# Performance work log

Hardware: AMD Instinct MI355X
Metric: run time of the kernel (lower is better)

## Reference

```python
import jax, jax.numpy as jnp
import numpy as np
from jax import lax

# Quantization bit-widths per the module: QuantAct(16) on input,
# QuantConv2d(precision[0]=8), QuantAct(precision[0]+3=11) after relu1,
# QuantLinear(precision[1]=8).
INPUT_BIT = 16
CONV_W_BIT = 8
RELU_BIT = 11
DENSE_W_BIT = 8
EPS = 1e-8


def round_ste(x):
    # straight-through estimator rounding (HAWQ SymmetricQuantFunction)
    return x + lax.stop_gradient(jnp.round(x) - x)


def quant_act(x, bit):
    """Per-tensor symmetric dynamic activation quantization (HAWQ QuantAct).
    Returns fake-quantized x and its scaling factor."""
    n = 2 ** (bit - 1) - 1
    scale = lax.stop_gradient(jnp.maximum(jnp.max(jnp.abs(x)), EPS) / n)
    x_q = jnp.clip(round_ste(x / scale), -n, n) * scale
    return x_q, scale


def quant_weight(w, bit):
    """Per-output-channel symmetric weight quantization. w: [out, ...].
    Returns integer-valued weights and per-channel scale [out]."""
    n = 2 ** (bit - 1) - 1
    absmax = jnp.max(jnp.abs(w.reshape(w.shape[0], -1)), axis=1)
    sf = lax.stop_gradient(jnp.maximum(absmax, EPS) / n)
    bshape = (w.shape[0],) + (1,) * (w.ndim - 1)
    w_int = jnp.clip(round_ste(w / sf.reshape(bshape)), -n, n)
    return w_int, sf


def quant_conv2d(x, p_sf, w, b, bit, stride, pad):
    w_int, w_sf = quant_weight(w, bit)          # [O,I,kh,kw], [O]
    x_int = x / p_sf                            # integer-valued activations
    out_int = lax.conv_general_dilated(
        x_int, w_int, window_strides=(stride, stride),
        padding=((pad, pad), (pad, pad)),
        dimension_numbers=("NCHW", "OIHW", "NCHW"))
    bias_sf = p_sf * w_sf                       # [O]
    b_int = round_ste(b / bias_sf)
    out = (out_int + b_int[None, :, None, None]) * bias_sf[None, :, None, None]
    return out, w_sf


def quant_linear(x, p_sf, w, b, bit):
    w_int, w_sf = quant_weight(w, bit)          # [O,I], [O]
    x_int = x / p_sf
    bias_sf = p_sf * w_sf                       # [O]
    b_int = round_ste(b / bias_sf)
    out = (jnp.einsum("bi,oi->bo", x_int, w_int) + b_int[None, :]) * bias_sf[None, :]
    return out


def setup_inputs() -> dict:
    key = jax.random.key(0)
    k1, k2, k3, k4, k5 = jax.random.split(key, 5)
    B, Cin, H, W = 256, 3, 64, 64
    Cout, K = 64, 3
    Fin, Fout = Cout * 32 * 32, 256  # stride-2 conv -> 32x32 spatial
    x = jax.random.normal(k1, (B, Cin, H, W), dtype=jnp.float32)
    conv_w = jax.random.normal(k2, (Cout, Cin, K, K), dtype=jnp.float32) * 0.1
    conv_b = jax.random.normal(k3, (Cout,), dtype=jnp.float32) * 0.01
    dense_w = jax.random.normal(k4, (Fout, Fin), dtype=jnp.float32) * 0.02
    dense_b = jax.random.normal(k5, (Fout,), dtype=jnp.float32) * 0.01
    return {"x": x, "conv_w": conv_w, "conv_b": conv_b,
            "dense_w": dense_w, "dense_b": dense_b}


def reference(x, conv_w, conv_b, dense_w, dense_b):
    # x, p_sf = quant_input(x)
    xq, p_sf = quant_act(x, INPUT_BIT)
    # x, w_sf = conv(x, p_sf)
    h, w_sf = quant_conv2d(xq, p_sf, conv_w, conv_b, CONV_W_BIT, stride=2, pad=1)
    # relu1
    h = jax.nn.relu(h)
    # x, p_sf = quant_relu(x, p_sf, w_sf)  (requantize at relu_bit)
    h, p_sf = quant_act(h, RELU_BIT)
    # flatten
    h = h.reshape(h.shape[0], -1)
    # relu2(enc_dense(x, p_sf))
    out = jax.nn.relu(quant_linear(h, p_sf, dense_w, dense_b, DENSE_W_BIT))
    return out
```

## Files before the change

kernel.cpp:

```cpp
#include <hip/hip_runtime.h>
#include <hip/hip_fp16.h>
#include <cstdint>

#define B_   256
#define CIN  3
#define HW_  64
#define COUT 64
#define FIN  65536
#define FOUT 256

#define ACC_F    0
#define SC_F     65536
#define XPART_F  65552
#define WPART_F  66064
#define CSF_F    67088
#define CWINT_F  67152
#define H16_BYTE (512*1024)
#define WQ_BYTE  (H16_BYTE + 256ll*FIN*2)

typedef _Float16 half8  __attribute__((ext_vector_type(8)));
typedef _Float16 half4v __attribute__((ext_vector_type(4)));
typedef float    floatx4 __attribute__((ext_vector_type(4)));
typedef unsigned short u16;
typedef unsigned int uint_;

__device__ inline float blockMax(float v) {
    #pragma unroll
    for (int off = 32; off; off >>= 1) v = fmaxf(v, __shfl_down(v, off));
    __shared__ float sm[8];
    const int lane = threadIdx.x & 63, w = threadIdx.x >> 6;
    if (lane == 0) sm[w] = v;
    __syncthreads();
    float m = sm[0];
    const int nw = blockDim.x >> 6;
    for (int i = 1; i < nw; i++) m = fmaxf(m, sm[i]);
    return m;
}

__global__ __launch_bounds__(256) void k_stats(const float* __restrict__ x,
                                               const float* __restrict__ dw,
                                               const float* __restrict__ cw,
                                               float* __restrict__ ws,
                                               signed char* __restrict__ wq) {
    const int b = blockIdx.x;
    const int t = threadIdx.x;
    if (b < 512) {
        const float4* x4 = (const float4*)x;
        float m = 0.f;
        for (int i = b * 256 + t; i < (B_ * CIN * HW_ * HW_) / 4; i += 512 * 256) {
            float4 v = x4[i];
            m = fmaxf(m, fmaxf(fmaxf(fabsf(v.x), fabsf(v.y)), fmaxf(fabsf(v.z), fabsf(v.w))));
        }
        float bm = blockMax(m);
        if (t == 0) ws[XPART_F + b] = bm;
    } else if (b < 768) {
        const int row = b - 512;
        const float4* r4 = (const float4*)(dw + (size_t)row * FIN);
        float m = 0.f;
        for (int i = t; i < FIN / 4; i += 256) {
            float4 v = r4[i];
            m = fmaxf(m, fmaxf(fmaxf(fabsf(v.x), fabsf(v.y)), fmaxf(fabsf(v.z), fabsf(v.w))));
        }
        const float am = blockMax(m);
        if (t == 0) ws[WPART_F + row] = am;
        const float inv = 127.0f / fmaxf(am, 1e-8f);
        uint_* wrow = (uint_*)(wq + (size_t)row * FIN);
        for (int i = t; i < FIN / 4; i += 256) {
            float4 v = r4[i];
            int q0 = (int)fminf(127.f, fmaxf(-127.f, rintf(v.x * inv)));
            int q1 = (int)fminf(127.f, fmaxf(-127.f, rintf(v.y * inv)));
            int q2 = (int)fminf(127.f, fmaxf(-127.f, rintf(v.z * inv)));
            int q3 = (int)fminf(127.f, fmaxf(-127.f, rintf(v.w * inv)));
            wrow[i] = (uint_)(q0 & 255) | ((uint_)(q1 & 255) << 8) |
                      ((uint_)(q2 & 255) << 16) | ((uint_)(q3 & 255) << 24);
        }
    } else if (b == 768) {
        if (t == 64) ((unsigned*)ws)[SC_F + 1] = 0u;
        if (t < 64) {
            const int o = t;
            float wv[27];
            float m = 0.f;
            #pragma unroll
            for (int i = 0; i < 27; i++) { wv[i] = cw[o * 27 + i]; m = fmaxf(m, fabsf(wv[i])); }
            const float sf = fmaxf(m, 1e-8f) / 127.0f;
            #pragma unroll
            for (int i = 0; i < 27; i++)
                ws[CWINT_F + o * 27 + i] = fminf(127.f, fmaxf(-127.f, rintf(wv[i] / sf)));
            ws[CSF_F + o] = sf;
        }
    } else {
        ws[ACC_F + (b - 769) * 256 + t] = 0.f;
    }
}

__global__ __launch_bounds__(256) void k_conv(const float* __restrict__ x,
                                              const float* __restrict__ cb,
                                              const float* __restrict__ ws,
                                              u16* __restrict__ h16,
                                              unsigned* __restrict__ maxh) {
    __shared__ float s_bsf[64], s_bint[64];
    __shared__ float xt[27 * 68];
    __shared__ float xp[256 * 28];
    const int t = threadIdx.x;

    float pm = fmaxf(ws[XPART_F + t], ws[XPART_F + 256 + t]);
    pm = blockMax(pm);
    const float p_sf = fmaxf(pm, 1e-8f) / 32767.0f;
    const float inv_p = 1.0f / p_sf;
    if (t < 64) {
        const float bsf = p_sf * ws[CSF_F + t];
        s_bsf[t]  = bsf;
        s_bint[t] = rintf(cb[t] / bsf);
    }

    const int b   = blockIdx.x >> 3;
    const int oyt = (blockIdx.x & 7) * 4;
    const float* xb = x + (size_t)b * (CIN * HW_ * HW_);

    for (int i = t; i < 432; i += 256) {
        const int lrow = i >> 4, c4 = i & 15;
        const int ci = lrow / 9, lr = lrow - ci * 9;
        const int iy = 2 * oyt - 1 + lr;
        float4 v = make_float4(0.f, 0.f, 0.f, 0.f);
        if ((unsigned)iy < 64u) v = *(const float4*)(xb + (ci * HW_ + iy) * HW_ + c4 * 4);
        float* d = &xt[lrow * 68 + 1 + c4 * 4];
        d[0] = fminf(32767.f, fmaxf(-32767.f, rintf(v.x * inv_p)));
        d[1] = fminf(32767.f, fmaxf(-32767.f, rintf(v.y * inv_p)));
        d[2] = fminf(32767.f, fmaxf(-32767.f, rintf(v.z * inv_p)));
        d[3] = fminf(32767.f, fmaxf(-32767.f, rintf(v.w * inv_p)));
    }
    if (t < 27) xt[t * 68] = 0.f;
    else if (t < 54) xt[(t - 27) * 68 + 65] = 0.f;
    __syncthreads();

    const int ox = t & 31;
    const int ch = __builtin_amdgcn_readfirstlane((t >> 6) & 1);
    const int dy = ((t >> 7) << 1) + ((t >> 5) & 1);
    const int oy = oyt + dy;

    float* myp = &xp[t * 28];
    #pragma unroll
    for (int ci = 0; ci < 3; ci++)
        #pragma unroll
        for (int ky = 0; ky < 3; ky++) {
            const float* rowp = &xt[(ci * 9 + 2 * dy + ky) * 68 + 2 * ox];
            #pragma unroll
            for (int kx = 0; kx < 3; kx++)
                myp[ci * 9 + ky * 3 + kx] = rowp[kx];
        }
    floatx4 xv0 = *(const floatx4*)(myp + 0);
    floatx4 xv1 = *(const floatx4*)(myp + 4);
    floatx4 xv2 = *(const floatx4*)(myp + 8);
    floatx4 xv3 = *(const floatx4*)(myp + 12);
    floatx4 xv4 = *(const floatx4*)(myp + 16);
    floatx4 xv5 = *(const floatx4*)(myp + 20);
    floatx4 xv6 = *(const floatx4*)(myp + 24);
    asm volatile("" : "+v"(xv0), "+v"(xv1), "+v"(xv2), "+v"(xv3),
                      "+v"(xv4), "+v"(xv5), "+v"(xv6));
    float xs[27];
    #pragma unroll
    for (int k = 0; k < 27; k++) {
        const int q = k >> 2, r = k & 3;
        xs[k] = (q == 0) ? xv0[r] : (q == 1) ? xv1[r] : (q == 2) ? xv2[r] :
                (q == 3) ? xv3[r] : (q == 4) ? xv4[r] : (q == 5) ? xv5[r] : xv6[r];
    }

    const float* wr = ws + CWINT_F + ch * (32 * 27);
    float mx = 0.f;
    u16* outp = h16 + (size_t)b * FIN + (size_t)ch * 32 * 1024 + oy * 32 + ox;

    float wbuf[27];
    #pragma unroll
    for (int k = 0; k < 27; k++) wbuf[k] = wr[k];
    #pragma unroll
    for (int c = 0; c < 32; c++) {
        float wcur[27];
        #pragma unroll
        for (int k = 0; k < 27; k++) wcur[k] = wbuf[k];
        if (c < 31) {
            const float* wn = wr + (c + 1) * 27;
            #pragma unroll
            for (int k = 0; k < 27; k++) wbuf[k] = wn[k];
        }
        float a = 0.f;
        #pragma unroll
        for (int k = 0; k < 27; k++) a = fmaf(xs[k], wcur[k], a);
        const int co = ch * 32 + c;
        float h = (a + s_bint[co]) * s_bsf[co];
        h = fmaxf(h, 0.f);
        mx = fmaxf(mx, h);
        outp[(size_t)c * 1024] = __half_as_ushort(__float2half(h));
    }
    float bm = blockMax(mx);
    if (t == 0) atomicMax(maxh, __float_as_uint(bm));
}

__device__ __forceinline__ half8 cvt_b8(uint_ lo, uint_ hi) {
    half8 h;
    h[0] = (_Float16)(float)(int)(signed char)(lo);
    h[1] = (_Float16)(float)(int)(signed char)(lo >> 8);
    h[2] = (_Float16)(float)(int)(signed char)(lo >> 16);
    h[3] = (_Float16)(float)(int)(signed char)(lo >> 24);
    h[4] = (_Float16)(float)(int)(signed char)(hi);
    h[5] = (_Float16)(float)(int)(signed char)(hi >> 8);
    h[6] = (_Float16)(float)(int)(signed char)(hi >> 16);
    h[7] = (_Float16)(float)(int)(signed char)(hi >> 24);
    return h;
}

__global__ __launch_bounds__(256) void k_gemm(const u16* __restrict__ h16,
                                              const signed char* __restrict__ wq,
                                              const float* __restrict__ ws,
                                              float* __restrict__ accb) {
    __shared__ __align__(16) _Float16 As[128][72];
    __shared__ __align__(16) _Float16 Bs[128][72];

    const int tid = threadIdx.x;
    const int tm  = (blockIdx.x >> 1) * 128;
    const int tn  = (blockIdx.x & 1) * 128;
    const int k0  = blockIdx.y * 1024;

    const float max_h  = __uint_as_float(((const unsigned*)ws)[SC_F + 1]);
    const float p2     = fmaxf(max_h, 1e-8f) / 1023.0f;
    const float inv_p2 = 1.0f / p2;

    floatx4 acc[4][4];
    const floatx4 zz = {0.f, 0.f, 0.f, 0.f};
    #pragma unroll
    for (int i = 0; i < 4; i++)
        #pragma unroll
        for (int j = 0; j < 4; j++) acc[i][j] = zz;

    const int wv = tid >> 6, lane = tid & 63;
    const int wm = (wv >> 1) * 64, wn = (wv & 1) * 64;
    const int lm = lane & 15, quad = lane >> 4;

    const int arow = tid >> 3, acol = tid & 7;
    const int brow = tid >> 1, bq   = (tid & 1) * 32;
    const u16* abase = h16 + (size_t)(tm + arow) * FIN + k0 + acol * 8;
    const signed char* bbase = wq + (size_t)(tn + brow) * FIN + k0 + bq;

#define LOADA(dst, kk) { _Pragma("unroll") \
    for (int r = 0; r < 4; r++) \
        dst[r] = *(const half8*)(abase + (size_t)r * 32 * FIN + (kk) * 64); }
#define LOADB(dst, kk) { const uint4* p_ = (const uint4*)(bbase + (kk) * 64); \
    dst[0] = p_[0]; dst[1] = p_[1]; }
#define STAGEA(src) { _Pragma("unroll") \
    for (int r = 0; r < 4; r++) { half8 qv; _Pragma("unroll") \
        for (int j = 0; j < 8; j++) { float f_ = (float)src[r][j]; \
            qv[j] = (_Float16)fminf(1023.f, rintf(f_ * inv_p2)); } \
        *(half8*)&As[arow + r * 32][acol * 8] = qv; } }
#define STAGEB(src) { _Pragma("unroll") \
    for (int u = 0; u < 2; u++) { uint4 wd_ = src[u]; \
        *(half8*)&Bs[brow][bq + u * 16 + 0] = cvt_b8(wd_.x, wd_.y); \
        *(half8*)&Bs[brow][bq + u * 16 + 8] = cvt_b8(wd_.z, wd_.w); } }
#define BARRIER() do { asm volatile("s_waitcnt lgkmcnt(0)" ::: "memory"); \
    __builtin_amdgcn_s_barrier(); } while (0)
#define MFMA_PHASE() { _Pragma("unroll") \
    for (int ks = 0; ks < 2; ks++) { half8 af[4], bf[4]; _Pragma("unroll") \
        for (int mi = 0; mi < 4; mi++) \
            af[mi] = *(const half8*)&As[wm + mi * 16 + lm][ks * 32 + quad * 8]; \
        _Pragma("unroll") \
        for (int ni = 0; ni < 4; ni++) \
            bf[ni] = *(const half8*)&Bs[wn + ni * 16 + lm][ks * 32 + quad * 8]; \
        _Pragma("unroll") \
        for (int mi = 0; mi < 4; mi++) _Pragma("unroll") \
            for (int ni = 0; ni < 4; ni++) \
                acc[mi][ni] = __builtin_amdgcn_mfma_f32_16x16x32_f16(af[mi], bf[ni], acc[mi][ni], 0, 0, 0); } }

    half8 a0[4], a1[4];
    uint4 b0[2], b1[2];

    LOADA(a0, 0); LOADB(b0, 0);
    LOADA(a1, 1); LOADB(b1, 1);

    for (int it = 0; it < 8; ++it) {
        STAGEA(a0); STAGEB(b0);
        if (it < 7) { LOADA(a0, 2 * it + 2); LOADB(b0, 2 * it + 2); }
        BARRIER();
        MFMA_PHASE();
        BARRIER();
        STAGEA(a1); STAGEB(b1);
        if (it < 7) { LOADA(a1, 2 * it + 3); LOADB(b1, 2 * it + 3); }
        BARRIER();
        MFMA_PHASE();
        BARRIER();
    }

    #pragma unroll
    for (int mi = 0; mi < 4; mi++)
        #pragma unroll
        for (int ni = 0; ni < 4; ni++)
            #pragma unroll
            for (int r = 0; r < 4; r++) {
                const int row = tm + wm + mi * 16 + quad * 4 + r;
                const int col = tn + wn + ni * 16 + lm;
                atomicAdd(accb + row * FOUT + col, acc[mi][ni][r]);
            }
#undef LOADA
#undef LOADB
#undef STAGEA
#undef STAGEB
#undef BARRIER
#undef MFMA_PHASE
}

__global__ void k_epi(const float* __restrict__ accb, const float* __restrict__ db,
                      const float* __restrict__ ws, float* __restrict__ out) {
    const int idx = blockIdx.x * 256 + threadIdx.x;
    const int n = idx & 255;
    const float max_h = __uint_as_float(((const unsigned*)ws)[SC_F + 1]);
    const float p2 = fmaxf(max_h, 1e-8f) / 1023.0f;
    const float am = fmaxf(ws[WPART_F + n], 1e-8f);
    const float wsf = am / 127.0f;
    const float bsf = p2 * wsf;
    const float bint = rintf(db[n] / bsf);
    out[idx] = fmaxf(0.f, (accb[idx] + bint) * bsf);
}

extern "C" void kernel_launch(void* const* d_in, const int* in_sizes, int n_in,
                              void* d_out, int out_size, void* d_ws, size_t ws_size,
                              hipStream_t stream) {
    (void)in_sizes; (void)n_in; (void)out_size; (void)ws_size;
    const float* x  = (const float*)d_in[0];
    const float* cw = (const float*)d_in[1];
    const float* cb = (const float*)d_in[2];
    const float* dw = (const float*)d_in[3];
    const float* db = (const float*)d_in[4];
    float* out = (float*)d_out;
    float* ws  = (float*)d_ws;
    u16* h16   = (u16*)((char*)d_ws + H16_BYTE);
    signed char* wq = (signed char*)d_ws + WQ_BYTE;
    float* accb = ws + ACC_F;
    unsigned* maxh = (unsigned*)ws + SC_F + 1;

    k_stats<<<1025, 256, 0, stream>>>(x, dw, cw, ws, wq);
    k_conv<<<2048, 256, 0, stream>>>(x, cb, ws, h16, maxh);
    k_gemm<<<dim3(4, 64), 256, 0, stream>>>(h16, wq, ws, accb);
    k_epi<<<256, 256, 0, stream>>>(accb, db, ws, out);
}
```

Before: 209.2 us.

## Split dense-weight absmax into quarter rows and move int8 quantization into conv launch

The per-row absmax of the dense weight is now computed by four blocks per row, each covering a quarter of the row, instead of one block per row. The epilogue and the quantizer combine the four partial maxima. The int8 quantization pass moves from the stats kernel into extra blocks appended to the conv kernel's grid. This replaces the long serial per-block loops over 256 KB rows with more and shorter blocks, and lets quantization run alongside the conv work. The cost is an extra combine step and a larger partial-max buffer in the workspace.

```diff
diff --git a/kernel.cpp b/kernel.cpp
--- a/kernel.cpp
+++ b/kernel.cpp
@@ -40,8 +40,7 @@
 __global__ __launch_bounds__(256) void k_stats(const float* __restrict__ x,
                                                const float* __restrict__ dw,
                                                const float* __restrict__ cw,
-                                               float* __restrict__ ws,
-                                               signed char* __restrict__ wq) {
+                                               float* __restrict__ ws) {
     const int b = blockIdx.x;
     const int t = threadIdx.x;
     if (b < 512) {
@@ -53,19 +52,53 @@
         }
         float bm = blockMax(m);
         if (t == 0) ws[XPART_F + b] = bm;
-    } else if (b < 768) {
-        const int row = b - 512;
-        const float4* r4 = (const float4*)(dw + (size_t)row * FIN);
+    } else if (b < 1536) {
+        const int b2 = b - 512;
+        const int row = b2 >> 2, q = b2 & 3;
+        const float4* r = (const float4*)(dw + (size_t)row * FIN) + q * 4096;
         float m = 0.f;
-        for (int i = t; i < FIN / 4; i += 256) {
-            float4 v = r4[i];
+        for (int i = t; i < 4096; i += 256) {
+            float4 v = r[i];
             m = fmaxf(m, fmaxf(fmaxf(fabsf(v.x), fabsf(v.y)), fmaxf(fabsf(v.z), fabsf(v.w))));
         }
-        const float am = blockMax(m);
-        if (t == 0) ws[WPART_F + row] = am;
+        float bm = blockMax(m);
+        if (t == 0) ws[WPART_F + b2] = bm;
+    } else if (b == 1536) {
+        if (t == 64) ((unsigned*)ws)[SC_F + 1] = 0u;
+        if (t < 64) {
+            const int o = t;
+            float wv[27];
+            float m = 0.f;
+            #pragma unroll
+            for (int i = 0; i < 27; i++) { wv[i] = cw[o * 27 + i]; m = fmaxf(m, fabsf(wv[i])); }
+            const float sf = fmaxf(m, 1e-8f) / 127.0f;
+            #pragma unroll
+            for (int i = 0; i < 27; i++)
+                ws[CWINT_F + o * 27 + i] = fminf(127.f, fmaxf(-127.f, rintf(wv[i] / sf)));
+            ws[CSF_F + o] = sf;
+        }
+    } else {
+        ws[ACC_F + (b - 1537) * 256 + t] = 0.f;
+    }
+}
+
+__global__ __launch_bounds__(256) void k_conv(const float* __restrict__ x,
+                                              const float* __restrict__ dw,
+                                              const float* __restrict__ cb,
+                                              const float* __restrict__ ws,
+                                              u16* __restrict__ h16,
+                                              signed char* __restrict__ wq,
+                                              unsigned* __restrict__ maxh) {
+    const int t = threadIdx.x;
+    if (blockIdx.x >= 2048) {
+        const int b2 = blockIdx.x - 2048;
+        const int row = b2 >> 2, q = b2 & 3;
+        const float* wp = ws + WPART_F + row * 4;
+        const float am = fmaxf(fmaxf(wp[0], wp[1]), fmaxf(wp[2], wp[3]));
         const float inv = 127.0f / fmaxf(am, 1e-8f);
-        uint_* wrow = (uint_*)(wq + (size_t)row * FIN);
-        for (int i = t; i < FIN / 4; i += 256) {
+        const float4* r4 = (const float4*)(dw + (size_t)row * FIN) + q * 4096;
+        uint_* wrow = (uint_*)(wq + (size_t)row * FIN) + q * 4096;
+        for (int i = t; i < 4096; i += 256) {
             float4 v = r4[i];
             int q0 = (int)fminf(127.f, fmaxf(-127.f, rintf(v.x * inv)));
             int q1 = (int)fminf(127.f, fmaxf(-127.f, rintf(v.y * inv)));
@@ -74,34 +107,12 @@
             wrow[i] = (uint_)(q0 & 255) | ((uint_)(q1 & 255) << 8) |
                       ((uint_)(q2 & 255) << 16) | ((uint_)(q3 & 255) << 24);
         }
-    } else if (b == 768) {
-        if (t == 64) ((unsigned*)ws)[SC_F + 1] = 0u;
-        if (t < 64) {
-            const int o = t;
-            float wv[27];
-            float m = 0.f;
-            #pragma unroll
-            for (int i = 0; i < 27; i++) { wv[i] = cw[o * 27 + i]; m = fmaxf(m, fabsf(wv[i])); }
-            const float sf = fmaxf(m, 1e-8f) / 127.0f;
-            #pragma unroll
-            for (int i = 0; i < 27; i++)
-                ws[CWINT_F + o * 27 + i] = fminf(127.f, fmaxf(-127.f, rintf(wv[i] / sf)));
-            ws[CSF_F + o] = sf;
-        }
-    } else {
-        ws[ACC_F + (b - 769) * 256 + t] = 0.f;
-    }
-}
-
-__global__ __launch_bounds__(256) void k_conv(const float* __restrict__ x,
-                                              const float* __restrict__ cb,
-                                              const float* __restrict__ ws,
-                                              u16* __restrict__ h16,
-                                              unsigned* __restrict__ maxh) {
+        return;
+    }
+
     __shared__ float s_bsf[64], s_bint[64];
     __shared__ float xt[27 * 68];
     __shared__ float xp[256 * 28];
-    const int t = threadIdx.x;
 
     float pm = fmaxf(ws[XPART_F + t], ws[XPART_F + 256 + t]);
     pm = blockMax(pm);
@@ -311,7 +322,8 @@
     const int n = idx & 255;
     const float max_h = __uint_as_float(((const unsigned*)ws)[SC_F + 1]);
     const float p2 = fmaxf(max_h, 1e-8f) / 1023.0f;
-    const float am = fmaxf(ws[WPART_F + n], 1e-8f);
+    const float* wp = ws + WPART_F + (size_t)n * 4;
+    const float am = fmaxf(fmaxf(fmaxf(wp[0], wp[1]), fmaxf(wp[2], wp[3])), 1e-8f);
     const float wsf = am / 127.0f;
     const float bsf = p2 * wsf;
     const float bint = rintf(db[n] / bsf);
@@ -334,8 +346,8 @@
     float* accb = ws + ACC_F;
     unsigned* maxh = (unsigned*)ws + SC_F + 1;
 
-    k_stats<<<1025, 256, 0, stream>>>(x, dw, cw, ws, wq);
-    k_conv<<<2048, 256, 0, stream>>>(x, cb, ws, h16, maxh);
+    k_stats<<<1793, 256, 0, stream>>>(x, dw, cw, ws);
+    k_conv<<<3072, 256, 0, stream>>>(x, dw, cb, ws, h16, wq, maxh);
     k_gemm<<<dim3(4, 64), 256, 0, stream>>>(h16, wq, ws, accb);
     k_epi<<<256, 256, 0, stream>>>(accb, db, ws, out);
 }
```

After: 191.0 us. 1.1x faster.
